# Performance work log

Measured on AMD Instinct MI355X. Metric: run time of the kernel, lower is better.

Reference implementation:

```python
import jax, jax.numpy as jnp
import numpy as np

N = 50000   # nodes
E = 800000  # edges
G = 64      # graphs in batch
H1, D1 = 2, 64   # gat1: 2 heads x 64
D2 = 32          # gat2: 1 head x 32
IN = 1
EPS = 1e-5


def _gat(h, src, dst, W, al, ar, Wres, bias, Hh, D):
    # DGL GATConv (eval mode): project, per-edge attention, edge softmax over dst, scatter-sum, residual + bias
    feat = (h @ W).reshape(N, Hh, D)                     # [N,H,D]
    el = jnp.sum(feat * al, axis=-1)                     # [N,H]
    er = jnp.sum(feat * ar, axis=-1)                     # [N,H]
    e = jax.nn.leaky_relu(el[src] + er[dst], 0.2)        # [E,H]
    m = jax.ops.segment_max(e, dst, num_segments=N)      # [N,H] (stable softmax)
    a = jnp.exp(e - m[dst])
    s = jax.ops.segment_sum(a, dst, num_segments=N)
    alpha = a / s[dst]                                   # [E,H]
    msg = feat[src] * alpha[:, :, None]                  # [E,H,D]
    rst = jax.ops.segment_sum(msg, dst, num_segments=N)  # [N,H,D]
    res = (h @ Wres).reshape(N, Hh, D)
    return rst + res + bias.reshape(1, Hh, D)


def _bn(x, gamma, beta, mean, var):
    return (x - mean) * jax.lax.rsqrt(var + EPS) * gamma + beta


def setup_inputs() -> dict:
    key = jax.random.key(0)
    ks = jax.random.split(key, 32)
    rn = lambda i, shape: jax.random.normal(ks[i], shape, jnp.float32) * 0.1
    inp = {
        'feat': jax.random.normal(ks[0], (N, IN), jnp.float32),
        'W1': rn(1, (IN, H1 * D1)), 'al1': rn(2, (H1, D1)), 'ar1': rn(3, (H1, D1)),
        'res1': rn(4, (IN, H1 * D1)), 'b1': rn(5, (H1 * D1,)),
        'g1_gamma': jnp.ones((H1 * D1,), jnp.float32), 'g1_beta': jnp.zeros((H1 * D1,), jnp.float32),
        'g1_mean': rn(6, (H1 * D1,)), 'g1_var': jax.random.uniform(ks[7], (H1 * D1,), jnp.float32) + 0.5,
        'W2': rn(8, (H1 * D1, D2)), 'al2': rn(9, (1, D2)), 'ar2': rn(10, (1, D2)),
        'res2': rn(11, (H1 * D1, D2)), 'b2': rn(12, (D2,)),
        'g2_gamma': jnp.ones((D2,), jnp.float32), 'g2_beta': jnp.zeros((D2,), jnp.float32),
        'g2_mean': rn(13, (D2,)), 'g2_var': jax.random.uniform(ks[14], (D2,), jnp.float32) + 0.5,
        'Wd1': rn(15, (D2, H1 * D1)), 'bd1': rn(16, (H1 * D1,)),
        'gd_gamma': jnp.ones((H1 * D1,), jnp.float32), 'gd_beta': jnp.zeros((H1 * D1,), jnp.float32),
        'gd_mean': rn(17, (H1 * D1,)), 'gd_var': jax.random.uniform(ks[18], (H1 * D1,), jnp.float32) + 0.5,
        'Wd2': rn(19, (H1 * D1, IN)), 'bd2': rn(20, (IN,)),
        'src': jax.random.randint(ks[21], (E,), 0, N, jnp.int32),
        'dst': jax.random.randint(ks[22], (E,), 0, N, jnp.int32),
        'graph_ids': jnp.sort(jax.random.randint(ks[23], (N,), 0, G, jnp.int32)),
    }
    return inp


def reference(feat, W1, al1, ar1, res1, b1, g1_gamma, g1_beta, g1_mean, g1_var,
              W2, al2, ar2, res2, b2, g2_gamma, g2_beta, g2_mean, g2_var,
              Wd1, bd1, gd_gamma, gd_beta, gd_mean, gd_var, Wd2, bd2,
              src, dst, graph_ids):
    h = _gat(feat, src, dst, W1, al1, ar1, res1, b1, H1, D1)   # [N,2,64]
    h = h.reshape(N, H1 * D1)
    h = jax.nn.relu(_bn(h, g1_gamma, g1_beta, g1_mean, g1_var))
    h = _gat(h, src, dst, W2, al2, ar2, res2, b2, 1, D2)       # [N,1,32]
    h = h.reshape(N, D2)
    h = jax.nn.relu(_bn(h, g2_gamma, g2_beta, g2_mean, g2_var))
    # dgl.mean_nodes over batched graphs
    counts = jax.ops.segment_sum(jnp.ones((N,), h.dtype), graph_ids, num_segments=G)
    graph_rep = jax.ops.segment_sum(h, graph_ids, num_segments=G) / jnp.maximum(counts, 1.0)[:, None]
    # decoder: Linear -> BN -> ReLU -> Linear (dropout off in eval)
    d = jax.nn.relu(_bn(h @ Wd1 + bd1, gd_gamma, gd_beta, gd_mean, gd_var))
    reconstruction = d @ Wd2 + bd2
    return graph_rep, reconstruction
```

## Files before the change

kernel.cpp:

```cpp
#include <hip/hip_runtime.h>
#include <hip/hip_bf16.h>
#include <hip/hip_fp16.h>

#define NN 50000
#define NE 800000
#define NG 64
#define C1 128
#define D2 32
#define CAP 32
#define RNG 6250
#define NCH 391
#define BN_EPS 1e-5f
#define PREP_BLOCKS 2048

#define CST_A   0
#define CST_B   2
#define CST_P   4
#define CST_Q   132
#define CST_R   260
#define CST_SC2 388
#define CST_RC2 420
#define CST_SD  452
#define CST_RD  580
#define CST_N   1024

#define UO_DEGP  0
#define UO_OVFC  800000
#define UO_WK    800016
#define ZERO_UNITS 800144
#define UO_FLAG  800144
#define UO_CST   800160
#define UO_ESRC2 801184
#define UO_OVF   1601184
#define UO_FCAN  3201184
#define UO_F2    3251184
#define UO_RS2   4051184
#define UO_EL2   5651184
#define UO_ER2   5701184
#define UO_END   5751184

typedef _Float16 h2vec __attribute__((ext_vector_type(2)));

__device__ __forceinline__ float lrelu(float x) { return fmaxf(x, 0.2f * x); }
__device__ __forceinline__ float bu2f(unsigned int u) {
    union { unsigned int i; float f; } v; v.i = (u & 0xFFFFu) << 16; return v.f;
}
__device__ __forceinline__ unsigned short f2bu(float f) {
    union { float f; unsigned int i; } v; v.f = f;
    unsigned int r = v.i + 0x7FFFu + ((v.i >> 16) & 1u);
    return (unsigned short)(r >> 16);
}
__device__ __forceinline__ unsigned int packh2(float a, float b) {
    h2vec h; h.x = (_Float16)a; h.y = (_Float16)b;
    union { h2vec h; unsigned int u; } v; v.h = h; return v.u;
}
__device__ __forceinline__ h2vec as_h2(unsigned int u) {
    union { unsigned int u; h2vec h; } v; v.u = u; return v.h;
}
__device__ __forceinline__ float ldw(const void* p, int i, int bf) {
    return bf ? bu2f(((const unsigned short*)p)[i]) : ((const float*)p)[i];
}
__device__ __forceinline__ int sniff64(const unsigned int* fw, int l) {
    int cnt = 0;
    for (int j = l; j < 256; j += 64) {
        unsigned int b = (fw[j] >> 8) & 0x7Fu;
        cnt += (b >= 0x3Au && b <= 0x41u) ? 1 : 0;
    }
#pragma unroll
    for (int m = 32; m >= 1; m >>= 1) cnt += __shfl_xor(cnt, m);
    return (cnt > 128) ? 1 : 0;
}

__global__ __launch_bounds__(256) void k_prep(
                       const void* __restrict__ feat, const int* __restrict__ dst,
                       const int* __restrict__ src,
                       float* __restrict__ fcan, int* __restrict__ degp,
                       unsigned short* __restrict__ esrc2,
                       int2* __restrict__ ovf, int* __restrict__ ovfc,
                       int* __restrict__ wk,
                       const void* W1, const void* al1, const void* ar1,
                       const void* res1, const void* b1,
                       const void* g1g, const void* g1b, const void* g1m, const void* g1v,
                       const void* b2v, const void* g2g, const void* g2b,
                       const void* g2m, const void* g2v,
                       const void* bd1, const void* gdg, const void* gdb,
                       const void* gdm, const void* gdv,
                       int* __restrict__ flag, float* __restrict__ cst) {
    __shared__ int sBf;
    __shared__ int sC;
    int t = threadIdx.x;
    if (t < 64) {
        int b = sniff64((const unsigned int*)feat, t);
        if (t == 0) sBf = b;
    }
    __syncthreads();
    int bf = sBf;

    if (blockIdx.x == 0) {
        if (t == 0) *flag = bf;
        if (t < 128) {
            if (t < 2) {
                float a = 0.0f, b = 0.0f;
                for (int d = 0; d < 64; ++d) {
                    float w = ldw(W1, t * 64 + d, bf);
                    a += w * ldw(al1, t * 64 + d, bf);
                    b += w * ldw(ar1, t * 64 + d, bf);
                }
                cst[CST_A + t] = a;
                cst[CST_B + t] = b;
            }
            {
                float sc = rsqrtf(ldw(g1v, t, bf) + BN_EPS) * ldw(g1g, t, bf);
                cst[CST_P + t] = ldw(W1, t, bf) * sc;
                cst[CST_Q + t] = ldw(res1, t, bf) * sc;
                cst[CST_R + t] = (ldw(b1, t, bf) - ldw(g1m, t, bf)) * sc + ldw(g1b, t, bf);
            }
            if (t < D2) {
                float sc = rsqrtf(ldw(g2v, t, bf) + BN_EPS) * ldw(g2g, t, bf);
                cst[CST_SC2 + t] = sc;
                cst[CST_RC2 + t] = (ldw(b2v, t, bf) - ldw(g2m, t, bf)) * sc + ldw(g2b, t, bf);
            }
            {
                float sc = rsqrtf(ldw(gdv, t, bf) + BN_EPS) * ldw(gdg, t, bf);
                cst[CST_SD + t] = sc;
                cst[CST_RD + t] = (ldw(bd1, t, bf) - ldw(gdm, t, bf)) * sc + ldw(gdb, t, bf);
            }
        }
    }

    for (int k = blockIdx.x * 256 + t; k < NN; k += PREP_BLOCKS * 256)
        fcan[k] = ldw(feat, k, bf);

    int xcc;
    asm volatile("s_getreg_b32 %0, hwreg(HW_REG_XCC_ID)" : "=s"(xcc));
    xcc &= 7;

    for (int rr = 0; rr < 8; ++rr) {
        int r = (xcc + rr) & 7;
        int lo = r * RNG, hi = lo + RNG;
        for (;;) {
            if (t == 0) sC = atomicAdd(&wk[r * 16], 1);
            __syncthreads();
            int c = sC;
            __syncthreads();
            if (c >= NCH) break;
#pragma unroll
            for (int j = 0; j < 8; ++j) {
                int k = c * 2048 + j * 256 + t;
                if (k < NE) {
                    int d = dst[k];
                    if (d >= lo && d < hi) {
                        int slot = atomicAdd(&degp[d << 4], 1);
                        if (slot < CAP) {
                            esrc2[d * CAP + slot] = (unsigned short)src[k];
                        } else {
                            int p = atomicAdd(ovfc, 1);
                            ovf[p] = make_int2(d, src[k]);
                        }
                    }
                }
            }
        }
    }
}

__global__ __launch_bounds__(256) void k_layer1(
        const float* __restrict__ fcan, const void* W2, const void* res2,
        const void* al2, const void* ar2,
        const int* __restrict__ flag, const float* __restrict__ cst,
        const int* __restrict__ degp, const unsigned short* __restrict__ esrc2,
        const int2* __restrict__ ovf, const int* __restrict__ ovfc,
        unsigned short* __restrict__ F2, float* __restrict__ RS2,
        float* __restrict__ EL2, float* __restrict__ ER2) {
    __shared__ unsigned int sW2pk[32 * 66];
    __shared__ unsigned int sR2pk[32 * 66];
    __shared__ unsigned int sH1pk[32 * 66];
    __shared__ float sP[C1], sQ[C1], sR[C1];
    __shared__ float sAl[D2], sAr[D2];
    int t = threadIdx.x;
    int bf = *flag;
    for (int u = t; u < 2048; u += 256) {
        int cw = u >> 5, l2 = u & 31;
        sW2pk[l2 * 66 + cw] = packh2(ldw(W2, cw * D2 + l2, bf),
                                     ldw(W2, (cw + 64) * D2 + l2, bf));
        sR2pk[l2 * 66 + cw] = packh2(ldw(res2, cw * D2 + l2, bf),
                                     ldw(res2, (cw + 64) * D2 + l2, bf));
    }
    if (t < C1) { sP[t] = cst[CST_P + t]; sQ[t] = cst[CST_Q + t]; sR[t] = cst[CST_R + t]; }
    if (t < D2) { sAl[t] = ldw(al2, t, bf); sAr[t] = ldw(ar2, t, bf); }
    __syncthreads();

    int l = t & 31;
    int g = t >> 5;
    int base = blockIdx.x * 32;
    float A0 = cst[CST_A + 0], A1 = cst[CST_A + 1];
    float B0 = cst[CST_B + 0], B1 = cst[CST_B + 1];

    int dcap[4], draw[4];
    float fiK[4];
#pragma unroll
    for (int k = 0; k < 4; ++k) {
        int i = base + g * 4 + k;
        if (i < NN) {
            draw[k] = degp[i << 4];
            dcap[k] = draw[k] < CAP ? draw[k] : CAP;
            fiK[k] = fcan[i];
        } else { draw[k] = 0; dcap[k] = 0; fiK[k] = 0.0f; }
    }
    float S0[4], S1[4], N0[4], N1[4];
#pragma unroll
    for (int k = 0; k < 4; ++k) { S0[k] = S1[k] = N0[k] = N1[k] = 0.0f; }
    int sA[4];
#pragma unroll
    for (int k = 0; k < 4; ++k)
        sA[k] = (l < dcap[k]) ? (int)esrc2[(base + g * 4 + k) * CAP + l] : 0;
    float fA[4];
#pragma unroll
    for (int k = 0; k < 4; ++k) fA[k] = fcan[sA[k]];
#pragma unroll
    for (int k = 0; k < 4; ++k) {
        if (l < dcap[k]) {
            float w0 = __expf(lrelu(A0 * fA[k] + B0 * fiK[k]));
            float w1 = __expf(lrelu(A1 * fA[k] + B1 * fiK[k]));
            S0[k] += w0; N0[k] += w0 * fA[k];
            S1[k] += w1; N1[k] += w1 * fA[k];
        }
    }
#pragma unroll
    for (int k = 0; k < 4; ++k) {
        if (draw[k] > CAP) {
            int i = base + g * 4 + k;
            int novf = *ovfc;
            for (int p = l; p < novf; p += 32) {
                int2 o = ovf[p];
                if (o.x == i) {
                    float fs = fcan[o.y];
                    float w0 = __expf(lrelu(A0 * fs + B0 * fiK[k]));
                    float w1 = __expf(lrelu(A1 * fs + B1 * fiK[k]));
                    S0[k] += w0; N0[k] += w0 * fs;
                    S1[k] += w1; N1[k] += w1 * fs;
                }
            }
        }
    }
#pragma unroll
    for (int m = 16; m >= 1; m >>= 1) {
#pragma unroll
        for (int k = 0; k < 4; ++k) {
            S0[k] += __shfl_xor(S0[k], m); N0[k] += __shfl_xor(N0[k], m);
            S1[k] += __shfl_xor(S1[k], m); N1[k] += __shfl_xor(N1[k], m);
        }
    }
#pragma unroll
    for (int k = 0; k < 4; ++k) {
        int slot = g * 4 + k;
        float T0 = S0[k] > 0.0f ? N0[k] / S0[k] : 0.0f;
        float T1 = S1[k] > 0.0f ? N1[k] / S1[k] : 0.0f;
        float h0  = fmaxf(sP[l]      * T0 + sQ[l]      * fiK[k] + sR[l],      0.0f);
        float h1v = fmaxf(sP[l + 32] * T0 + sQ[l + 32] * fiK[k] + sR[l + 32], 0.0f);
        float h2v = fmaxf(sP[l + 64] * T1 + sQ[l + 64] * fiK[k] + sR[l + 64], 0.0f);
        float h3v = fmaxf(sP[l + 96] * T1 + sQ[l + 96] * fiK[k] + sR[l + 96], 0.0f);
        sH1pk[slot * 66 + l]      = packh2(h0,  h2v);
        sH1pk[slot * 66 + l + 32] = packh2(h1v, h3v);
    }
    __syncthreads();

    int w = t >> 6;
    int half = (t >> 5) & 1;
    int nb0 = w * 8 + half * 4;
    float aF[4] = {0.f, 0.f, 0.f, 0.f}, aR[4] = {0.f, 0.f, 0.f, 0.f};
    for (int cw = 0; cw < 64; cw += 2) {
        uint2 wq = *(const uint2*)&sW2pk[l * 66 + cw];
        uint2 rq = *(const uint2*)&sR2pk[l * 66 + cw];
#pragma unroll
        for (int n = 0; n < 4; ++n) {
            uint2 hq = *(const uint2*)&sH1pk[(nb0 + n) * 66 + cw];
            aF[n] = __builtin_amdgcn_fdot2(as_h2(hq.x), as_h2(wq.x),
                    __builtin_amdgcn_fdot2(as_h2(hq.y), as_h2(wq.y), aF[n], false), false);
            aR[n] = __builtin_amdgcn_fdot2(as_h2(hq.x), as_h2(rq.x),
                    __builtin_amdgcn_fdot2(as_h2(hq.y), as_h2(rq.y), aR[n], false), false);
        }
    }
#pragma unroll
    for (int n = 0; n < 4; ++n) {
        int i = base + nb0 + n;
        if (i < NN) {
            float elp = aF[n] * sAl[l], erp = aF[n] * sAr[l];
#pragma unroll
            for (int m = 16; m >= 1; m >>= 1) {
                elp += __shfl_xor(elp, m);
                erp += __shfl_xor(erp, m);
            }
            if (l == 0) { EL2[i] = elp; ER2[i] = erp; }
            F2[(size_t)i * D2 + l]  = f2bu(aF[n]);
            RS2[(size_t)i * D2 + l] = aR[n];
        }
    }
}

__global__ __launch_bounds__(256, 8) void k_final(
        const void* Wd1, const void* Wd2, const void* bd2,
        const int* __restrict__ flag, const float* __restrict__ cst,
        const int* __restrict__ degp, const unsigned short* __restrict__ esrc2,
        const int2* __restrict__ ovf, const int* __restrict__ ovfc,
        const unsigned short* __restrict__ F2, float* __restrict__ RS2,
        const float* __restrict__ EL2, const float* __restrict__ ER2,
        float* __restrict__ out) {
    __shared__ float sWd1x[4096];
    __shared__ unsigned int sWS[8 * 64];
    int t = threadIdx.x;
    int bf = *flag;
    for (int u = t; u < 4096; u += 256) {
        int d = u >> 7, lq = (u >> 2) & 31, j = u & 3;
        sWd1x[u] = ldw(Wd1, d * C1 + j * 32 + lq, bf);
    }

    int i = (blockIdx.x * 256 + t) >> 5;
    int l = t & 31;
    int nb = t >> 5;

    float sc2 = cst[CST_SC2 + l], rc2 = cst[CST_RC2 + l];
    float sd0 = cst[CST_SD + l],      rd0 = cst[CST_RD + l];
    float sd1 = cst[CST_SD + l + 32], rd1 = cst[CST_RD + l + 32];
    float sd2 = cst[CST_SD + l + 64], rd2 = cst[CST_RD + l + 64];
    float sd3 = cst[CST_SD + l + 96], rd3 = cst[CST_RD + l + 96];
    float wd2_0 = ldw(Wd2, l, bf),      wd2_1 = ldw(Wd2, l + 32, bf);
    float wd2_2 = ldw(Wd2, l + 64, bf), wd2_3 = ldw(Wd2, l + 96, bf);
    __syncthreads();

    float eri = ER2[i];
    int dr = degp[i << 4];
    int dcap = dr < CAP ? dr : CAP;
    const unsigned short* row = &esrc2[i * CAP];

    int sMy = 0; float wMy = 0.0f;
    if (l < dcap) {
        sMy = (int)row[l];
        wMy = __expf(lrelu(EL2[sMy] + eri));
    }
    float S = wMy;
#pragma unroll
    for (int m = 16; m >= 1; m >>= 1) S += __shfl_xor(S, m);
    sWS[nb * 64 + 2 * l]     = __float_as_uint(wMy);
    sWS[nb * 64 + 2 * l + 1] = (unsigned int)sMy;

    float aF0 = 0.f, aF1 = 0.f, aF2 = 0.f, aF3 = 0.f;
    int e = 0;
    for (; e + 3 < dcap; e += 4) {
        uint2 p0 = *(const uint2*)&sWS[nb * 64 + 2 * e];
        uint2 p1 = *(const uint2*)&sWS[nb * 64 + 2 * (e + 1)];
        uint2 p2 = *(const uint2*)&sWS[nb * 64 + 2 * (e + 2)];
        uint2 p3 = *(const uint2*)&sWS[nb * 64 + 2 * (e + 3)];
        float v0 = bu2f(F2[(size_t)p0.y * D2 + l]);
        float v1 = bu2f(F2[(size_t)p1.y * D2 + l]);
        float v2 = bu2f(F2[(size_t)p2.y * D2 + l]);
        float v3 = bu2f(F2[(size_t)p3.y * D2 + l]);
        aF0 = fmaf(__uint_as_float(p0.x), v0, aF0);
        aF1 = fmaf(__uint_as_float(p1.x), v1, aF1);
        aF2 = fmaf(__uint_as_float(p2.x), v2, aF2);
        aF3 = fmaf(__uint_as_float(p3.x), v3, aF3);
    }
    for (; e < dcap; ++e) {
        uint2 p = *(const uint2*)&sWS[nb * 64 + 2 * e];
        aF0 = fmaf(__uint_as_float(p.x), bu2f(F2[(size_t)p.y * D2 + l]), aF0);
    }
    if (dr > CAP) {
        int novf = *ovfc;
        for (int p = 0; p < novf; ++p) {
            int2 o = ovf[p];
            if (o.x == i) {
                float wA = __expf(lrelu(EL2[o.y] + eri));
                S += wA;
                aF0 = fmaf(wA, bu2f(F2[(size_t)o.y * D2 + l]), aF0);
            }
        }
    }
    float aF = (aF0 + aF1) + (aF2 + aF3);
    float inv = S > 0.0f ? 1.0f / S : 0.0f;

    float h2 = fmaxf((aF * inv + RS2[(size_t)i * D2 + l]) * sc2 + rc2, 0.0f);
    RS2[(size_t)i * D2 + l] = h2;

    const float4* Wx = (const float4*)sWd1x;
    float ac0 = 0.0f, ac1 = 0.0f, ac2 = 0.0f, ac3 = 0.0f;
#pragma unroll
    for (int d = 0; d < D2; ++d) {
        float h = __shfl(h2, d, 32);
        float4 wv = Wx[d * 32 + l];
        ac0 = fmaf(h, wv.x, ac0);
        ac1 = fmaf(h, wv.y, ac1);
        ac2 = fmaf(h, wv.z, ac2);
        ac3 = fmaf(h, wv.w, ac3);
    }
    float rec = fmaxf(ac0 * sd0 + rd0, 0.0f) * wd2_0
              + fmaxf(ac1 * sd1 + rd1, 0.0f) * wd2_1
              + fmaxf(ac2 * sd2 + rd2, 0.0f) * wd2_2
              + fmaxf(ac3 * sd3 + rd3, 0.0f) * wd2_3;
#pragma unroll
    for (int m = 16; m >= 1; m >>= 1) rec += __shfl_xor(rec, m);
    if (l == 0) out[NG * D2 + i] = rec + ldw(bd2, 0, bf);
}

__global__ __launch_bounds__(256) void k_pool2(const int* __restrict__ gid,
                                               const float* __restrict__ H2,
                                               float* __restrict__ out) {
    __shared__ int sLo, sHi;
    __shared__ float sAcc[32 * 32];
    int g = blockIdx.x >> 2;
    int part = blockIdx.x & 3;
    int t = threadIdx.x;
    if (t == 0) {
        int lo = 0, hi = NN;
        while (lo < hi) { int m = (lo + hi) >> 1; if (gid[m] < g) lo = m + 1; else hi = m; }
        sLo = lo;
        lo = 0; hi = NN;
        while (lo < hi) { int m = (lo + hi) >> 1; if (gid[m] < g + 1) lo = m + 1; else hi = m; }
        sHi = lo;
    }
    __syncthreads();
    int lo = sLo, hi = sHi;
    int q = t & 7;
    int row = t >> 3;
    float4 acc = make_float4(0.f, 0.f, 0.f, 0.f);
    for (int i = lo + part * 32 + row; i < hi; i += 128) {
        float4 v = ((const float4*)&H2[(size_t)i * D2])[q];
        acc.x += v.x; acc.y += v.y; acc.z += v.z; acc.w += v.w;
    }
    *(float4*)&sAcc[row * 32 + 4 * q] = acc;
    __syncthreads();
    if (t < 32) {
        float a = 0.0f;
        for (int r = 0; r < 32; ++r) a += sAcc[r * 32 + t];
        float inv = 1.0f / fmaxf((float)(hi - lo), 1.0f);
        atomicAdd(&out[g * D2 + t], a * inv);
    }
}

extern "C" void kernel_launch(void* const* d_in, const int* in_sizes, int n_in,
                              void* d_out, int out_size, void* d_ws, size_t ws_size,
                              hipStream_t stream) {
    const void* feat = d_in[0];
    const void* W1 = d_in[1];  const void* al1 = d_in[2];  const void* ar1 = d_in[3];
    const void* res1 = d_in[4]; const void* b1 = d_in[5];
    const void* g1g = d_in[6]; const void* g1b = d_in[7];
    const void* g1m = d_in[8]; const void* g1v = d_in[9];
    const void* W2 = d_in[10]; const void* al2 = d_in[11]; const void* ar2 = d_in[12];
    const void* res2 = d_in[13]; const void* b2v = d_in[14];
    const void* g2g = d_in[15]; const void* g2b = d_in[16];
    const void* g2m = d_in[17]; const void* g2v = d_in[18];
    const void* Wd1 = d_in[19]; const void* bd1 = d_in[20];
    const void* gdg = d_in[21]; const void* gdb = d_in[22];
    const void* gdm = d_in[23]; const void* gdv = d_in[24];
    const void* Wd2 = d_in[25]; const void* bd2 = d_in[26];
    const int* src = (const int*)d_in[27];
    const int* dst = (const int*)d_in[28];
    const int* gid = (const int*)d_in[29];

    unsigned int* wsu = (unsigned int*)d_ws;
    int* degp   = (int*)(wsu + UO_DEGP);
    int* ovfc   = (int*)(wsu + UO_OVFC);
    int* wk     = (int*)(wsu + UO_WK);
    int* flag   = (int*)(wsu + UO_FLAG);
    float* cst  = (float*)(wsu + UO_CST);
    unsigned short* esrc2 = (unsigned short*)(wsu + UO_ESRC2);
    int2* ovf   = (int2*)(wsu + UO_OVF);
    float* fcan = (float*)(wsu + UO_FCAN);
    unsigned short* F2 = (unsigned short*)(wsu + UO_F2);
    float* RS2  = (float*)(wsu + UO_RS2);
    float* EL2  = (float*)(wsu + UO_EL2);
    float* ER2  = (float*)(wsu + UO_ER2);

    hipMemsetAsync(d_ws, 0, (size_t)ZERO_UNITS * 4, stream);
    hipMemsetAsync(d_out, 0, (size_t)NG * D2 * sizeof(float), stream);

    k_prep<<<PREP_BLOCKS, 256, 0, stream>>>(feat, dst, src, fcan, degp,
                                            esrc2, ovf, ovfc, wk,
                                            W1, al1, ar1, res1, b1,
                                            g1g, g1b, g1m, g1v,
                                            b2v, g2g, g2b, g2m, g2v,
                                            bd1, gdg, gdb, gdm, gdv,
                                            flag, cst);

    k_layer1<<<(NN + 31) / 32, 256, 0, stream>>>(fcan, W2, res2, al2, ar2, flag, cst,
                                                 degp, esrc2, ovf, ovfc,
                                                 F2, RS2, EL2, ER2);

    k_final<<<(NN * 32) / 256, 256, 0, stream>>>(Wd1, Wd2, bd2, flag, cst,
                                                 degp, esrc2, ovf, ovfc,
                                                 F2, RS2, EL2, ER2,
                                                 (float*)d_out);

    k_pool2<<<NG * 4, 256, 0, stream>>>(gid, RS2, (float*)d_out);
}
```

Measured before the change: 284.3 us.

## Replace atomic work-stealing CSR build with static grid over four dst ranges

The edge-bucketing prep kernel no longer uses XCC-aware atomic work stealing over eight destination ranges. It now launches a static grid of chunk-by-range blocks over four wider ranges, so each edge chunk is scanned four times instead of eight and the chunk-counter atomics go away. The W1·al1 and W1·ar1 reductions become wave shuffles. The pooling kernel uses one block per graph and writes results directly, which removes the output memset and the atomics. The trade-off is less L2 locality per range, because ranges no longer map to XCCs, and less parallelism in pooling.

```diff
diff --git a/kernel.cpp b/kernel.cpp
--- a/kernel.cpp
+++ b/kernel.cpp
@@ -8,10 +8,10 @@
 #define C1 128
 #define D2 32
 #define CAP 32
-#define RNG 6250
+#define NRANGE 4
+#define RNG 12500
 #define NCH 391
 #define BN_EPS 1e-5f
-#define PREP_BLOCKS 2048
 
 #define CST_A   0
 #define CST_B   2
@@ -26,18 +26,16 @@
 
 #define UO_DEGP  0
 #define UO_OVFC  800000
-#define UO_WK    800016
-#define ZERO_UNITS 800144
-#define UO_FLAG  800144
-#define UO_CST   800160
-#define UO_ESRC2 801184
-#define UO_OVF   1601184
-#define UO_FCAN  3201184
-#define UO_F2    3251184
-#define UO_RS2   4051184
-#define UO_EL2   5651184
-#define UO_ER2   5701184
-#define UO_END   5751184
+#define ZERO_UNITS 800016
+#define UO_FLAG  800016
+#define UO_CST   800032
+#define UO_ESRC2 801056
+#define UO_OVF   1601056
+#define UO_FCAN  3201056
+#define UO_F2    3251056
+#define UO_RS2   4051056
+#define UO_EL2   5651056
+#define UO_ER2   5701056
 
 typedef _Float16 h2vec __attribute__((ext_vector_type(2)));
 
@@ -77,7 +75,6 @@
                        float* __restrict__ fcan, int* __restrict__ degp,
                        unsigned short* __restrict__ esrc2,
                        int2* __restrict__ ovf, int* __restrict__ ovfc,
-                       int* __restrict__ wk,
                        const void* W1, const void* al1, const void* ar1,
                        const void* res1, const void* b1,
                        const void* g1g, const void* g1b, const void* g1m, const void* g1v,
@@ -87,7 +84,6 @@
                        const void* gdm, const void* gdv,
                        int* __restrict__ flag, float* __restrict__ cst) {
     __shared__ int sBf;
-    __shared__ int sC;
     int t = threadIdx.x;
     if (t < 64) {
         int b = sniff64((const unsigned int*)feat, t);
@@ -95,72 +91,50 @@
     }
     __syncthreads();
     int bf = sBf;
+    int r = blockIdx.x / NCH;
+    int c = blockIdx.x % NCH;
 
     if (blockIdx.x == 0) {
         if (t == 0) *flag = bf;
         if (t < 128) {
-            if (t < 2) {
-                float a = 0.0f, b = 0.0f;
-                for (int d = 0; d < 64; ++d) {
-                    float w = ldw(W1, t * 64 + d, bf);
-                    a += w * ldw(al1, t * 64 + d, bf);
-                    b += w * ldw(ar1, t * 64 + d, bf);
-                }
-                cst[CST_A + t] = a;
-                cst[CST_B + t] = b;
+            float w1v = ldw(W1, t, bf);
+            float pa = w1v * ldw(al1, t, bf);
+            float pb = w1v * ldw(ar1, t, bf);
+#pragma unroll
+            for (int m = 32; m >= 1; m >>= 1) { pa += __shfl_xor(pa, m); pb += __shfl_xor(pb, m); }
+            if ((t & 63) == 0) { cst[CST_A + (t >> 6)] = pa; cst[CST_B + (t >> 6)] = pb; }
+            float sc = rsqrtf(ldw(g1v, t, bf) + BN_EPS) * ldw(g1g, t, bf);
+            cst[CST_P + t] = w1v * sc;
+            cst[CST_Q + t] = ldw(res1, t, bf) * sc;
+            cst[CST_R + t] = (ldw(b1, t, bf) - ldw(g1m, t, bf)) * sc + ldw(g1b, t, bf);
+            if (t < D2) {
+                float s2 = rsqrtf(ldw(g2v, t, bf) + BN_EPS) * ldw(g2g, t, bf);
+                cst[CST_SC2 + t] = s2;
+                cst[CST_RC2 + t] = (ldw(b2v, t, bf) - ldw(g2m, t, bf)) * s2 + ldw(g2b, t, bf);
             }
-            {
-                float sc = rsqrtf(ldw(g1v, t, bf) + BN_EPS) * ldw(g1g, t, bf);
-                cst[CST_P + t] = ldw(W1, t, bf) * sc;
-                cst[CST_Q + t] = ldw(res1, t, bf) * sc;
-                cst[CST_R + t] = (ldw(b1, t, bf) - ldw(g1m, t, bf)) * sc + ldw(g1b, t, bf);
-            }
-            if (t < D2) {
-                float sc = rsqrtf(ldw(g2v, t, bf) + BN_EPS) * ldw(g2g, t, bf);
-                cst[CST_SC2 + t] = sc;
-                cst[CST_RC2 + t] = (ldw(b2v, t, bf) - ldw(g2m, t, bf)) * sc + ldw(g2b, t, bf);
-            }
-            {
-                float sc = rsqrtf(ldw(gdv, t, bf) + BN_EPS) * ldw(gdg, t, bf);
-                cst[CST_SD + t] = sc;
-                cst[CST_RD + t] = (ldw(bd1, t, bf) - ldw(gdm, t, bf)) * sc + ldw(gdb, t, bf);
-            }
-        }
-    }
-
-    for (int k = blockIdx.x * 256 + t; k < NN; k += PREP_BLOCKS * 256)
-        fcan[k] = ldw(feat, k, bf);
-
-    int xcc;
-    asm volatile("s_getreg_b32 %0, hwreg(HW_REG_XCC_ID)" : "=s"(xcc));
-    xcc &= 7;
-
-    for (int rr = 0; rr < 8; ++rr) {
-        int r = (xcc + rr) & 7;
-        int lo = r * RNG, hi = lo + RNG;
-        for (;;) {
-            if (t == 0) sC = atomicAdd(&wk[r * 16], 1);
-            __syncthreads();
-            int c = sC;
-            __syncthreads();
-            if (c >= NCH) break;
-#pragma unroll
-            for (int j = 0; j < 8; ++j) {
-                int k = c * 2048 + j * 256 + t;
-                if (k < NE) {
-                    int d = dst[k];
-                    if (d >= lo && d < hi) {
-                        int slot = atomicAdd(&degp[d << 4], 1);
-                        if (slot < CAP) {
-                            esrc2[d * CAP + slot] = (unsigned short)src[k];
-                        } else {
-                            int p = atomicAdd(ovfc, 1);
-                            ovf[p] = make_int2(d, src[k]);
-                        }
-                    }
+            float sd = rsqrtf(ldw(gdv, t, bf) + BN_EPS) * ldw(gdg, t, bf);
+            cst[CST_SD + t] = sd;
+            cst[CST_RD + t] = (ldw(bd1, t, bf) - ldw(gdm, t, bf)) * sd + ldw(gdb, t, bf);
+        }
+    }
+
+    int lo = r * RNG, hi = lo + RNG;
+#pragma unroll
+    for (int j = 0; j < 8; ++j) {
+        int k = c * 2048 + j * 256 + t;
+        if (k < NE) {
+            int d = dst[k];
+            if (d >= lo && d < hi) {
+                int slot = atomicAdd(&degp[d << 4], 1);
+                if (slot < CAP) {
+                    esrc2[d * CAP + slot] = (unsigned short)src[k];
+                } else {
+                    int p = atomicAdd(ovfc, 1);
+                    ovf[p] = make_int2(d, src[k]);
                 }
             }
         }
+        if (r == 0 && k < NN) fcan[k] = ldw(feat, k, bf);
     }
 }
 
@@ -406,8 +380,7 @@
                                                float* __restrict__ out) {
     __shared__ int sLo, sHi;
     __shared__ float sAcc[32 * 32];
-    int g = blockIdx.x >> 2;
-    int part = blockIdx.x & 3;
+    int g = blockIdx.x;
     int t = threadIdx.x;
     if (t == 0) {
         int lo = 0, hi = NN;
@@ -422,7 +395,7 @@
     int q = t & 7;
     int row = t >> 3;
     float4 acc = make_float4(0.f, 0.f, 0.f, 0.f);
-    for (int i = lo + part * 32 + row; i < hi; i += 128) {
+    for (int i = lo + row; i < hi; i += 32) {
         float4 v = ((const float4*)&H2[(size_t)i * D2])[q];
         acc.x += v.x; acc.y += v.y; acc.z += v.z; acc.w += v.w;
     }
@@ -431,8 +404,8 @@
     if (t < 32) {
         float a = 0.0f;
         for (int r = 0; r < 32; ++r) a += sAcc[r * 32 + t];
-        float inv = 1.0f / fmaxf((float)(hi - lo), 1.0f);
-        atomicAdd(&out[g * D2 + t], a * inv);
+        float c = (float)(hi - lo);
+        out[g * D2 + t] = a / fmaxf(c, 1.0f);
     }
 }
 
@@ -459,7 +432,6 @@
     unsigned int* wsu = (unsigned int*)d_ws;
     int* degp   = (int*)(wsu + UO_DEGP);
     int* ovfc   = (int*)(wsu + UO_OVFC);
-    int* wk     = (int*)(wsu + UO_WK);
     int* flag   = (int*)(wsu + UO_FLAG);
     float* cst  = (float*)(wsu + UO_CST);
     unsigned short* esrc2 = (unsigned short*)(wsu + UO_ESRC2);
@@ -471,15 +443,14 @@
     float* ER2  = (float*)(wsu + UO_ER2);
 
     hipMemsetAsync(d_ws, 0, (size_t)ZERO_UNITS * 4, stream);
-    hipMemsetAsync(d_out, 0, (size_t)NG * D2 * sizeof(float), stream);
-
-    k_prep<<<PREP_BLOCKS, 256, 0, stream>>>(feat, dst, src, fcan, degp,
-                                            esrc2, ovf, ovfc, wk,
-                                            W1, al1, ar1, res1, b1,
-                                            g1g, g1b, g1m, g1v,
-                                            b2v, g2g, g2b, g2m, g2v,
-                                            bd1, gdg, gdb, gdm, gdv,
-                                            flag, cst);
+
+    k_prep<<<NCH * NRANGE, 256, 0, stream>>>(feat, dst, src, fcan, degp,
+                                             esrc2, ovf, ovfc,
+                                             W1, al1, ar1, res1, b1,
+                                             g1g, g1b, g1m, g1v,
+                                             b2v, g2g, g2b, g2m, g2v,
+                                             bd1, gdg, gdb, gdm, gdv,
+                                             flag, cst);
 
     k_layer1<<<(NN + 31) / 32, 256, 0, stream>>>(fcan, W2, res2, al2, ar2, flag, cst,
                                                  degp, esrc2, ovf, ovfc,
@@ -490,5 +461,5 @@
                                                  F2, RS2, EL2, ER2,
                                                  (float*)d_out);
 
-    k_pool2<<<NG * 4, 256, 0, stream>>>(gid, RS2, (float*)d_out);
-}
+    k_pool2<<<NG, 256, 0, stream>>>(gid, RS2, (float*)d_out);
+}
```

Result: faster. 250.8 us (-11.8%).
